# Kernel optimization log

Measured on AMD Instinct MI355X. Metric: run time of the kernel, lower is better.

Reference implementation:

```python
import jax, jax.numpy as jnp
import numpy as np

EPS = 1e-5  # BatchNorm2d default eps


def _resize_bilinear(x, out_h, out_w):
    # PyTorch F.interpolate(mode='bilinear', align_corners=False, antialias=False):
    # input coord = (out + 0.5)/scale - 0.5  ->  translation = 0.5*(scale-1)
    b, c, h, w = x.shape
    sh, sw = out_h / h, out_w / w
    scale = jnp.array([sh, sw], dtype=jnp.float32)
    trans = jnp.array([0.5 * (sh - 1.0), 0.5 * (sw - 1.0)], dtype=jnp.float32)
    return jax.image.scale_and_translate(
        x, (b, c, out_h, out_w), (2, 3), scale, trans,
        method='linear', antialias=False)


def setup_inputs() -> dict:
    key = jax.random.key(0)
    ks = jax.random.split(key, 6)
    B, C, IC, H, W = 4, 64, 16, 128, 128
    init = lambda k, shape, fan_in: (
        jax.random.normal(k, shape, jnp.float32) / np.float32(np.sqrt(fan_in)))
    return {
        'x': jax.random.normal(ks[0], (B, C, H, W), jnp.float32),
        'g_w': init(ks[1], (IC, C), C), 'g_b': jnp.zeros((IC,), jnp.float32),
        'theta_w': init(ks[2], (IC, C), C), 'theta_b': jnp.zeros((IC,), jnp.float32),
        'phi_w': init(ks[3], (IC, C), C), 'phi_b': jnp.zeros((IC,), jnp.float32),
        'out_w': init(ks[4], (C, IC), IC), 'out_b': jnp.zeros((C,), jnp.float32),
        'bn_gamma': jnp.ones((C,), jnp.float32), 'bn_beta': jnp.zeros((C,), jnp.float32),
    }


def reference(x, g_w, g_b, theta_w, theta_b, phi_w, phi_b,
              out_w, out_b, bn_gamma, bn_beta):
    b, c, h, w = x.shape
    dh, dw = h // 2, w // 2          # downsample_factor = 0.5
    xd = _resize_bilinear(x, dh, dw).reshape(b, c, dh * dw)  # [b,C,N]

    # 1x1 convs == per-pixel linear projections
    g_x = jnp.einsum('bcn,oc->bno', xd, g_w) + g_b          # [b,N,IC]
    th = jnp.einsum('bcn,oc->bno', xd, theta_w) + theta_b   # [b,N,IC]
    ph = jnp.einsum('bcn,oc->bon', xd, phi_w) + phi_b[None, :, None]  # [b,IC,N]

    f = jnp.einsum('bni,bim->bnm', th, ph)   # [b,N,N] score matrix (no scaling)
    attn = jax.nn.softmax(f, axis=-1)
    y = jnp.einsum('bnm,bmi->bni', attn, g_x)               # [b,N,IC]
    y = y.transpose(0, 2, 1).reshape(b, -1, dh, dw)         # [b,IC,dh,dw]

    y = _resize_bilinear(y, h, w)                            # upsample back
    y = jnp.einsum('bihw,ci->bchw', y, out_w) + out_b[None, :, None, None]

    z = x + y
    # BatchNorm2d in (default) training mode: biased batch stats over (B,H,W)
    mean = jnp.mean(z, axis=(0, 2, 3))
    var = jnp.var(z, axis=(0, 2, 3))
    zn = (z - mean[None, :, None, None]) * jax.lax.rsqrt(var + EPS)[None, :, None, None]
    return zn * bn_gamma[None, :, None, None] + bn_beta[None, :, None, None]
```

## Files before the change

### kernel.cpp

```cpp
#include <hip/hip_runtime.h>
#include <math.h>

#define NB 4
#define NC 64
#define NI 16
#define NH 128
#define NW 128
#define ND 64
#define NN 4096
#define KSPL 4

#define LOG2E 1.4426950408889634f

using bfrag  = __attribute__((ext_vector_type(8))) short;
using bfrag4 = __attribute__((ext_vector_type(4))) short;
using ffrag  = __attribute__((ext_vector_type(4))) float;

#if __has_builtin(__builtin_amdgcn_exp2f)
#define EXP2(x) __builtin_amdgcn_exp2f(x)
#else
#define EXP2(x) exp2f(x)
#endif

__device__ __forceinline__ unsigned bf16rne(float f) {
    unsigned u = __float_as_uint(f);
    return (u + 0x7FFFu + ((u >> 16) & 1u)) >> 16;
}
__device__ __forceinline__ unsigned pk_rne(float lo, float hi) {
    return bf16rne(lo) | (bf16rne(hi) << 16);
}
__device__ __forceinline__ unsigned pk_trunc(float lo, float hi) {
    return (__float_as_uint(lo) >> 16) | (__float_as_uint(hi) & 0xFFFF0000u);
}

__device__ __forceinline__ ffrag mfma_qk(bfrag4 a, bfrag4 b, ffrag c) {
#if __has_builtin(__builtin_amdgcn_mfma_f32_16x16x16bf16_1k)
    return __builtin_amdgcn_mfma_f32_16x16x16bf16_1k(a, b, c, 0, 0, 0);
#else
    union { bfrag4 h[2]; bfrag v; } ua, ub;
    bfrag4 zz = {0, 0, 0, 0};
    ua.h[0] = a; ua.h[1] = zz;
    ub.h[0] = b; ub.h[1] = zz;
    return __builtin_amdgcn_mfma_f32_16x16x32_bf16(ua.v, ub.v, c, 0, 0, 0);
#endif
}

extern "C" __global__ __launch_bounds__(256)
void k_proj(const float* __restrict__ x,
            const float* __restrict__ gw, const float* __restrict__ gb,
            const float* __restrict__ tw, const float* __restrict__ tb,
            const float* __restrict__ pw, const float* __restrict__ pb,
            uint2* __restrict__ th_sw, uint2* __restrict__ phi_sw,
            uint4* __restrict__ g_sw, float* __restrict__ stats)
{
    __shared__ float swt[NC][48];
    __shared__ float sb[48];
    __shared__ float red[3][64][49];
    __shared__ __align__(16) unsigned short gtile[16][64];
    int tid = threadIdx.x;
    int b = blockIdx.x >> 6, i = blockIdx.x & 63;
    if (blockIdx.x == 0 && tid < 128) stats[tid] = 0.f;
    for (int idx = tid; idx < NI*NC; idx += 256) {
        int o = idx >> 6, c = idx & 63;
        swt[c][o]      = tw[idx];
        swt[c][16 + o] = pw[idx];
        swt[c][32 + o] = gw[idx];
    }
    if (tid < 16) { sb[tid] = tb[tid]; sb[16+tid] = pb[tid]; sb[32+tid] = gb[tid]; }
    __syncthreads();

    int j = tid & 63, part = tid >> 6;
    const float* xp = x + (((size_t)(b*NC + part*16))*NH + (2*i+1))*NW + (2*j+1);
    float a[48];
#pragma unroll
    for (int k = 0; k < 48; ++k) a[k] = 0.f;
    for (int cc = 0; cc < 16; ++cc) {
        float xd = xp[(size_t)cc*NH*NW];
        const float* wr = swt[part*16 + cc];
#pragma unroll
        for (int k = 0; k < 48; ++k) a[k] += xd*wr[k];
    }
    if (part != 0) {
#pragma unroll
        for (int k = 0; k < 48; ++k) red[part-1][j][k] = a[k];
    }
    __syncthreads();
    if (part == 0) {
        float aT[16], aP[16], aG[16];
#pragma unroll
        for (int o = 0; o < 16; ++o) {
            float vT = a[o]    + red[0][j][o]    + red[1][j][o]    + red[2][j][o];
            float vP = a[16+o] + red[0][j][16+o] + red[1][j][16+o] + red[2][j][16+o];
            float vG = a[32+o] + red[0][j][32+o] + red[1][j][32+o] + red[2][j][32+o];
            aT[o] = (vT + sb[o]) * LOG2E;
            aP[o] =  vP + sb[16+o];
            aG[o] =  vG + sb[32+o];
        }
        int q = i*64 + j;
        int n = j & 15;
        size_t qtile = (size_t)b*256 + (q >> 4);
#pragma unroll
        for (int qd = 0; qd < 4; ++qd)
            th_sw[qtile*64 + qd*16 + n] =
                make_uint2(pk_rne(aT[4*qd], aT[4*qd+1]), pk_rne(aT[4*qd+2], aT[4*qd+3]));
        int wk = j & 31;
        int f = (wk >> 2) & 1;
        int r = ((wk >> 3) << 2) | (wk & 3);
        size_t kgrp = (size_t)b*256 + (q >> 5)*2 + f;
#pragma unroll
        for (int qd = 0; qd < 4; ++qd)
            phi_sw[kgrp*64 + qd*16 + r] =
                make_uint2(pk_rne(aP[4*qd], aP[4*qd+1]), pk_rne(aP[4*qd+2], aP[4*qd+3]));
#pragma unroll
        for (int o = 0; o < 16; ++o) gtile[o][j] = (unsigned short)bf16rne(aG[o]);
    }
    __syncthreads();
    if (tid < 128) {
        int c2 = tid >> 6, L = tid & 63;
        int n = L & 15, q8 = L >> 4;
        const uint4* src = (const uint4*)&gtile[n][c2*32 + q8*8];
        g_sw[((size_t)b*128 + i*2 + c2)*64 + L] = *src;
    }
}

extern "C" __global__ __launch_bounds__(256, 4)
void k_attn(const uint2* __restrict__ th_sw, const uint2* __restrict__ phi_sw,
            const uint4* __restrict__ g_sw, float* __restrict__ accp,
            float* __restrict__ lp)
{
    __shared__ __align__(16) uint2 sphi[16*64];
    __shared__ __align__(16) uint4 sg[8*64];
    int tid = threadIdx.x;
    int wave = tid >> 6, lane = tid & 63;
    int quad = lane >> 4, low = lane & 15;
    int qgroup = blockIdx.x, ks = blockIdx.y, b = blockIdx.z;

    union { uint2 u; bfrag4 f; } thu;
    thu.u = th_sw[((size_t)b*256 + qgroup*4 + wave)*64 + lane];
    bfrag4 theta = thu.f;

    ffrag yacc = {0.f, 0.f, 0.f, 0.f};
    const ffrag zf = {0.f, 0.f, 0.f, 0.f};
    float lacc = 0.f;

    for (int chunk = 0; chunk < 4; ++chunk) {
        __syncthreads();
        const uint4* srcP = (const uint4*)(phi_sw + ((size_t)b*256 + ks*64 + chunk*16)*64);
        const uint4* srcG = g_sw + ((size_t)b*128 + ks*32 + chunk*8)*64;
        ((uint4*)sphi)[tid]       = srcP[tid];
        ((uint4*)sphi)[256 + tid] = srcP[256 + tid];
        sg[tid]       = srcG[tid];
        sg[256 + tid] = srcG[256 + tid];
        __syncthreads();

        const bfrag4* sphiF = (const bfrag4*)sphi;
        const bfrag*  sgF   = (const bfrag*)sg;
#pragma unroll
        for (int s = 0; s < 8; ++s) {
            bfrag4 pA = sphiF[(2*s+0)*64 + lane];
            bfrag4 pB = sphiF[(2*s+1)*64 + lane];
            bfrag  vf = sgF[s*64 + lane];
            ffrag sA = mfma_qk(pA, theta, zf);
            ffrag sB = mfma_qk(pB, theta, zf);
            float eA0 = EXP2(sA[0]), eA1 = EXP2(sA[1]), eA2 = EXP2(sA[2]), eA3 = EXP2(sA[3]);
            float eB0 = EXP2(sB[0]), eB1 = EXP2(sB[1]), eB2 = EXP2(sB[2]), eB3 = EXP2(sB[3]);
            lacc += ((eA0+eA1) + (eA2+eA3)) + ((eB0+eB1) + (eB2+eB3));
            union { unsigned u[4]; bfrag f; } pu;
            pu.u[0] = pk_trunc(eA0, eA1);
            pu.u[1] = pk_trunc(eA2, eA3);
            pu.u[2] = pk_trunc(eB0, eB1);
            pu.u[3] = pk_trunc(eB2, eB3);
            yacc = __builtin_amdgcn_mfma_f32_16x16x32_bf16(pu.f, vf, yacc, 0, 0, 0);
        }
    }

    lacc += __shfl_xor(lacc, 16, 64);
    lacc += __shfl_xor(lacc, 32, 64);

    int qbase = qgroup*64 + wave*16;
    size_t pbase = ((size_t)ks*NB + b)*NN;
#pragma unroll
    for (int reg = 0; reg < 4; ++reg)
        accp[(pbase + qbase + quad*4 + reg)*16 + low] = yacc[reg];
    if (lane < 16) lp[pbase + qbase + lane] = lacc;
}

extern "C" __global__ __launch_bounds__(256)
void k_outz(const float* __restrict__ accp, const float* __restrict__ lp,
            const float* __restrict__ x, const float* __restrict__ ow,
            const float* __restrict__ ob, float* __restrict__ z)
{
    __shared__ float syd[2][NI][ND];
    __shared__ float sl[2][ND];
    __shared__ float swv[NC*NI];
    __shared__ float sbv[NC];
    int t = threadIdx.x;
    int hp = blockIdx.x, b = blockIdx.y;
    for (int idx = t; idx < NC*NI; idx += 256) swv[idx] = ow[idx];
    if (t < NC) sbv[t] = ob[t];

    {
        int r = t >> 7, col = (t >> 1) & 63, half = t & 1;
        int row = (r == 0) ? (hp > 0 ? hp-1 : 0) : hp;
        int q = row*64 + col;
        float4 a0 = make_float4(0.f,0.f,0.f,0.f), a1 = a0;
        float lsum = 0.f;
        for (int ks = 0; ks < KSPL; ++ks) {
            const float4* ap = (const float4*)accp + (((size_t)ks*NB + b)*NN + q)*4 + 2*half;
            float4 v0 = ap[0], v1 = ap[1];
            a0.x += v0.x; a0.y += v0.y; a0.z += v0.z; a0.w += v0.w;
            a1.x += v1.x; a1.y += v1.y; a1.z += v1.z; a1.w += v1.w;
            if (half == 0) lsum += lp[((size_t)ks*NB + b)*NN + q];
        }
        if (half == 0) sl[r][col] = lsum;
        __syncthreads();
        float inv = 1.f / sl[r][col];
        int i0 = 8*half;
        syd[r][i0+0][col] = a0.x*inv; syd[r][i0+1][col] = a0.y*inv;
        syd[r][i0+2][col] = a0.z*inv; syd[r][i0+3][col] = a0.w*inv;
        syd[r][i0+4][col] = a1.x*inv; syd[r][i0+5][col] = a1.y*inv;
        syd[r][i0+6][col] = a1.z*inv; syd[r][i0+7][col] = a1.w*inv;
    }
    __syncthreads();

    int w = t & 127, hsel = t >> 7;
    int h = 2*hp + hsel;
    float wh0 = hsel ? 0.f : 0.5f;
    float wh1 = hsel ? 1.f : 0.5f;
    int c0, c1; float wc0, wc1;
    if (w & 1) { c0 = c1 = (w-1) >> 1; wc0 = 1.f; wc1 = 0.f; }
    else       { c1 = w >> 1; c0 = c1 ? c1-1 : 0; wc0 = 0.5f; wc1 = 0.5f; }
    float yv[16];
#pragma unroll
    for (int i = 0; i < 16; ++i)
        yv[i] = wh0*(wc0*syd[0][i][c0] + wc1*syd[0][i][c1])
              + wh1*(wc0*syd[1][i][c0] + wc1*syd[1][i][c1]);

    const float* xb = x + (((size_t)(b*NC))*NH + h)*NW + w;
    float* zb       = z + (((size_t)(b*NC))*NH + h)*NW + w;
    for (int c = 0; c < NC; ++c) {
        const float* wr = swv + c*16;
        float acc = sbv[c];
#pragma unroll
        for (int i = 0; i < 16; ++i) acc += wr[i]*yv[i];
        zb[(size_t)c*NH*NW] = xb[(size_t)c*NH*NW] + acc;
    }
}

extern "C" __global__ __launch_bounds__(256)
void k_stats(const float* __restrict__ z, float* __restrict__ stats)
{
    int c = blockIdx.x, b = blockIdx.y;
    const float4* zp = (const float4*)(z + ((size_t)(b*NC + c))*NH*NW);
    float s = 0.f, s2 = 0.f;
    for (int i = threadIdx.x; i < NH*NW/4; i += 256) {
        float4 v = zp[i];
        s  += v.x + v.y + v.z + v.w;
        s2 += v.x*v.x + v.y*v.y + v.z*v.z + v.w*v.w;
    }
#pragma unroll
    for (int off = 32; off > 0; off >>= 1) {
        s  += __shfl_down(s, off);
        s2 += __shfl_down(s2, off);
    }
    __shared__ float red[8];
    int lane = threadIdx.x & 63, wv = threadIdx.x >> 6;
    if (lane == 0) { red[wv] = s; red[4+wv] = s2; }
    __syncthreads();
    if (threadIdx.x == 0) {
        atomicAdd(&stats[c],    red[0]+red[1]+red[2]+red[3]);
        atomicAdd(&stats[NC+c], red[4]+red[5]+red[6]+red[7]);
    }
}

extern "C" __global__ __launch_bounds__(256)
void k_norm(const float* __restrict__ z, const float* __restrict__ stats,
            const float* __restrict__ gamma, const float* __restrict__ beta,
            float* __restrict__ out)
{
    size_t i4 = (size_t)blockIdx.x*256 + threadIdx.x;
    int c = (int)((i4 >> 12) & 63);
    const float inv_cnt = 1.f/65536.f;
    float mean = stats[c]*inv_cnt;
    float var  = stats[NC+c]*inv_cnt - mean*mean;
    float rs = rsqrtf(var + 1e-5f);
    float ga = gamma[c]*rs;
    float be = beta[c] - mean*ga;
    float4 v = ((const float4*)z)[i4];
    ((float4*)out)[i4] = make_float4(v.x*ga+be, v.y*ga+be, v.z*ga+be, v.w*ga+be);
}

extern "C" void kernel_launch(void* const* d_in, const int* in_sizes, int n_in,
                              void* d_out, int out_size, void* d_ws, size_t ws_size,
                              hipStream_t stream)
{
    const float* x     = (const float*)d_in[0];
    const float* gw    = (const float*)d_in[1];
    const float* gb    = (const float*)d_in[2];
    const float* tw    = (const float*)d_in[3];
    const float* tb    = (const float*)d_in[4];
    const float* pw    = (const float*)d_in[5];
    const float* pb    = (const float*)d_in[6];
    const float* ow    = (const float*)d_in[7];
    const float* ob    = (const float*)d_in[8];
    const float* gamma = (const float*)d_in[9];
    const float* beta  = (const float*)d_in[10];
    float* out = (float*)d_out;

    char* wsb = (char*)d_ws;
    uint2* th_sw  = (uint2*)(wsb);
    uint2* phi_sw = (uint2*)(wsb + (512u<<10));
    uint4* g_sw   = (uint4*)(wsb + (1024u<<10));
    float* lp     = (float*)(wsb + (1536u<<10));
    float* stats  = (float*)(wsb + (1792u<<10));
    float* accp   = (float*)(wsb + (2048u<<10));
    float* z      = (float*)(wsb + (6u<<20) + (256u<<10));

    k_proj <<<256, 256, 0, stream>>>(x, gw, gb, tw, tb, pw, pb,
                                     th_sw, phi_sw, g_sw, stats);
    k_attn <<<dim3(64, KSPL, NB), 256, 0, stream>>>(th_sw, phi_sw, g_sw, accp, lp);
    k_outz <<<dim3(64, NB), 256, 0, stream>>>(accp, lp, x, ow, ob, z);
    k_stats<<<dim3(NC, NB), 256, 0, stream>>>(z, stats);
    k_norm <<<4096, 256, 0, stream>>>(z, stats, gamma, beta, out);
}
```

Before: 130.3 us.

## Fuse BatchNorm statistics into output kernel with sharded atomics, drop stats pass

```diff
diff --git a/kernel.cpp b/kernel.cpp
--- a/kernel.cpp
+++ b/kernel.cpp
@@ -51,7 +51,7 @@
             const float* __restrict__ tw, const float* __restrict__ tb,
             const float* __restrict__ pw, const float* __restrict__ pb,
             uint2* __restrict__ th_sw, uint2* __restrict__ phi_sw,
-            uint4* __restrict__ g_sw, float* __restrict__ stats)
+            uint4* __restrict__ g_sw, float* __restrict__ shstats)
 {
     __shared__ float swt[NC][48];
     __shared__ float sb[48];
@@ -59,7 +59,10 @@
     __shared__ __align__(16) unsigned short gtile[16][64];
     int tid = threadIdx.x;
     int b = blockIdx.x >> 6, i = blockIdx.x & 63;
-    if (blockIdx.x == 0 && tid < 128) stats[tid] = 0.f;
+    if (blockIdx.x == 0) {
+#pragma unroll
+        for (int k = 0; k < 4; ++k) shstats[tid + k*256] = 0.f;
+    }
     for (int idx = tid; idx < NI*NC; idx += 256) {
         int o = idx >> 6, c = idx & 63;
         swt[c][o]      = tw[idx];
@@ -188,8 +191,10 @@
 extern "C" __global__ __launch_bounds__(256)
 void k_outz(const float* __restrict__ accp, const float* __restrict__ lp,
             const float* __restrict__ x, const float* __restrict__ ow,
-            const float* __restrict__ ob, float* __restrict__ z)
-{
+            const float* __restrict__ ob, float* __restrict__ z,
+            float* __restrict__ shstats)
+{
+    __shared__ float slab[32*257];
     __shared__ float syd[2][NI][ND];
     __shared__ float sl[2][ND];
     __shared__ float swv[NC*NI];
@@ -238,56 +243,71 @@
 
     const float* xb = x + (((size_t)(b*NC))*NH + h)*NW + w;
     float* zb       = z + (((size_t)(b*NC))*NH + h)*NW + w;
+    float zreg[64];
+#pragma unroll
     for (int c = 0; c < NC; ++c) {
         const float* wr = swv + c*16;
         float acc = sbv[c];
 #pragma unroll
         for (int i = 0; i < 16; ++i) acc += wr[i]*yv[i];
-        zb[(size_t)c*NH*NW] = xb[(size_t)c*NH*NW] + acc;
+        zreg[c] = xb[(size_t)c*NH*NW] + acc;
+        zb[(size_t)c*NH*NW] = zreg[c];
+    }
+
+    float* shadow = shstats + ((((unsigned)b << 6) + (unsigned)hp) & 7u)*128;
+    int c32 = t >> 3, oct = t & 7;
+#pragma unroll
+    for (int half = 0; half < 2; ++half) {
+        __syncthreads();
+#pragma unroll
+        for (int cc = 0; cc < 32; ++cc)
+            slab[cc*257 + t] = zreg[half*32 + cc];
+        __syncthreads();
+        float s = 0.f, s2 = 0.f;
+#pragma unroll
+        for (int k = 0; k < 32; ++k) {
+            int p2 = oct*32 + ((k + 4*oct) & 31);
+            float v = slab[c32*257 + p2];
+            s += v; s2 += v*v;
+        }
+        s  += __shfl_xor(s, 1);  s  += __shfl_xor(s, 2);  s  += __shfl_xor(s, 4);
+        s2 += __shfl_xor(s2, 1); s2 += __shfl_xor(s2, 2); s2 += __shfl_xor(s2, 4);
+        if (oct == 0) atomicAdd(shadow + half*32 + c32, s);
+        if (oct == 1) atomicAdd(shadow + 64 + half*32 + c32, s2);
     }
 }
 
 extern "C" __global__ __launch_bounds__(256)
-void k_stats(const float* __restrict__ z, float* __restrict__ stats)
-{
-    int c = blockIdx.x, b = blockIdx.y;
-    const float4* zp = (const float4*)(z + ((size_t)(b*NC + c))*NH*NW);
-    float s = 0.f, s2 = 0.f;
-    for (int i = threadIdx.x; i < NH*NW/4; i += 256) {
-        float4 v = zp[i];
-        s  += v.x + v.y + v.z + v.w;
-        s2 += v.x*v.x + v.y*v.y + v.z*v.z + v.w*v.w;
-    }
-#pragma unroll
-    for (int off = 32; off > 0; off >>= 1) {
-        s  += __shfl_down(s, off);
-        s2 += __shfl_down(s2, off);
-    }
-    __shared__ float red[8];
-    int lane = threadIdx.x & 63, wv = threadIdx.x >> 6;
-    if (lane == 0) { red[wv] = s; red[4+wv] = s2; }
-    __syncthreads();
-    if (threadIdx.x == 0) {
-        atomicAdd(&stats[c],    red[0]+red[1]+red[2]+red[3]);
-        atomicAdd(&stats[NC+c], red[4]+red[5]+red[6]+red[7]);
-    }
-}
-
-extern "C" __global__ __launch_bounds__(256)
-void k_norm(const float* __restrict__ z, const float* __restrict__ stats,
+void k_norm(const float* __restrict__ z, const float* __restrict__ shstats,
             const float* __restrict__ gamma, const float* __restrict__ beta,
             float* __restrict__ out)
 {
-    size_t i4 = (size_t)blockIdx.x*256 + threadIdx.x;
-    int c = (int)((i4 >> 12) & 63);
-    const float inv_cnt = 1.f/65536.f;
-    float mean = stats[c]*inv_cnt;
-    float var  = stats[NC+c]*inv_cnt - mean*mean;
-    float rs = rsqrtf(var + 1e-5f);
-    float ga = gamma[c]*rs;
-    float be = beta[c] - mean*ga;
-    float4 v = ((const float4*)z)[i4];
-    ((float4*)out)[i4] = make_float4(v.x*ga+be, v.y*ga+be, v.z*ga+be, v.w*ga+be);
+    __shared__ float sga[NC], sbe[NC];
+    int t = threadIdx.x;
+    if (t < NC) {
+        float s = 0.f, s2 = 0.f;
+#pragma unroll
+        for (int sh = 0; sh < 8; ++sh) {
+            s  += shstats[sh*128 + t];
+            s2 += shstats[sh*128 + 64 + t];
+        }
+        const float inv_cnt = 1.f/65536.f;
+        float mean = s*inv_cnt;
+        float var  = s2*inv_cnt - mean*mean;
+        float rs = rsqrtf(var + 1e-5f);
+        float ga = gamma[t]*rs;
+        sga[t] = ga;
+        sbe[t] = beta[t] - mean*ga;
+    }
+    __syncthreads();
+#pragma unroll
+    for (int it = 0; it < 4; ++it) {
+        size_t i4 = ((size_t)blockIdx.x*4 + it)*256 + t;
+        int c = (int)((i4 >> 12) & 63);
+        float4 v = ((const float4*)z)[i4];
+        float ga = sga[c], be = sbe[c];
+        ((float4*)out)[i4] = make_float4(v.x*ga+be, v.y*ga+be, v.z*ga+be, v.w*ga+be);
+    }
 }
 
 extern "C" void kernel_launch(void* const* d_in, const int* in_sizes, int n_in,
@@ -312,14 +332,13 @@
     uint2* phi_sw = (uint2*)(wsb + (512u<<10));
     uint4* g_sw   = (uint4*)(wsb + (1024u<<10));
     float* lp     = (float*)(wsb + (1536u<<10));
-    float* stats  = (float*)(wsb + (1792u<<10));
+    float* shst   = (float*)(wsb + (1792u<<10));
     float* accp   = (float*)(wsb + (2048u<<10));
     float* z      = (float*)(wsb + (6u<<20) + (256u<<10));
 
-    k_proj <<<256, 256, 0, stream>>>(x, gw, gb, tw, tb, pw, pb,
-                                     th_sw, phi_sw, g_sw, stats);
-    k_attn <<<dim3(64, KSPL, NB), 256, 0, stream>>>(th_sw, phi_sw, g_sw, accp, lp);
-    k_outz <<<dim3(64, NB), 256, 0, stream>>>(accp, lp, x, ow, ob, z);
-    k_stats<<<dim3(NC, NB), 256, 0, stream>>>(z, stats);
-    k_norm <<<4096, 256, 0, stream>>>(z, stats, gamma, beta, out);
-}
+    k_proj<<<256, 256, 0, stream>>>(x, gw, gb, tw, tb, pw, pb,
+                                    th_sw, phi_sw, g_sw, shst);
+    k_attn<<<dim3(64, KSPL, NB), 256, 0, stream>>>(th_sw, phi_sw, g_sw, accp, lp);
+    k_outz<<<dim3(64, NB), 256, 0, stream>>>(accp, lp, x, ow, ob, z, shst);
+    k_norm<<<1024, 256, 0, stream>>>(z, shst, gamma, beta, out);
+}
```

Result: faster. 127.0 us (-2.6%).
